# Performance work log

Hardware: AMD Instinct MI355X
Metric: run time of the kernel (lower is better)

The kernel has to match this reference:

```python
import jax, jax.numpy as jnp
import numpy as np

B, NTH, NTW, M, DF = 64, 56, 56, 8, 8
FAR = 100.0  # sentinel location for off sources, as in the torch module


def setup_inputs() -> dict:
    key = jax.random.key(0)
    k1, k2, k3, k4, k5 = jax.random.split(key, 5)
    est_locs = jax.random.uniform(k1, (B, NTH, NTW, M, 2), dtype=jnp.float32)
    true_locs = jax.random.uniform(k2, (B, NTH, NTW, M, 2), dtype=jnp.float32)
    true_fluxes = jax.random.normal(k3, (B, NTH, NTW, M, DF), dtype=jnp.float32)
    est_n_sources = jax.random.randint(k4, (B, NTH, NTW), 0, M + 1, dtype=jnp.int32)
    true_n_sources = jax.random.randint(k5, (B, NTH, NTW), 0, M + 1, dtype=jnp.int32)
    return {"est_locs": est_locs, "true_locs": true_locs, "true_fluxes": true_fluxes,
            "est_n_sources": est_n_sources, "true_n_sources": true_n_sources}


def reference(est_locs, true_locs, true_fluxes, est_n_sources, true_n_sources):
    b, nth, ntw, m, _ = est_locs.shape
    T = b * nth * ntw
    slot = jnp.arange(m)
    # is_on_mask per tile: first n_sources slots are on
    est_on = slot[None, :] < est_n_sources.reshape(T, 1)    # [T, m] bool
    true_on = slot[None, :] < true_n_sources.reshape(T, 1)  # [T, m] bool

    # masked locs -> pairwise L2 distances (torch.cdist p=2)
    el = jnp.where(est_on[..., None], est_locs.reshape(T, m, 2), jnp.float32(FAR))
    tl = jnp.where(true_on[..., None], true_locs.reshape(T, m, 2), jnp.float32(FAR))
    diff = el[:, :, None, :] - tl[:, None, :, :]
    dist = jnp.sqrt(jnp.sum(diff * diff, axis=-1))  # [T, m, m]

    # _fast_one_to_one_match
    match1 = jnp.argmin(dist, axis=1)  # best est row per true col  [T, m]
    match2 = jnp.argmin(dist, axis=2)  # best true col per est row  [T, m]
    match1cond2 = jnp.take_along_axis(match1, match2, axis=1)
    one2one = match1cond2 == slot[None, :]
    est_out = match1 > (est_on.sum(-1, keepdims=True) - 1)
    true_out = match2 > (true_on.sum(-1, keepdims=True) - 1)
    one2one = one2one & ~(est_out | true_out)
    # unmatched pairs point to the padded dump slot m (== est_to_true*mask + offset)
    est_idx = jnp.where(one2one, match1, m)
    true_idx = jnp.where(one2one, match2, m)

    # flat indices across (b*nth*ntw) tiles, each of width m+1
    tile_off = (jnp.arange(T) * (m + 1))[:, None]
    flat_est = (est_idx + tile_off).reshape(-1)
    flat_true = (true_idx + tile_off).reshape(-1)

    # padded true catalog: locs(2) | fluxes(DF) | n_sources-indicator(1)
    fields = jnp.concatenate([
        true_locs.reshape(T, m, 2),
        true_fluxes.reshape(T, m, -1),
        true_on[..., None].astype(jnp.float32),
    ], axis=-1)  # [T, m, 2+DF+1]
    d = fields.shape[-1]
    padded = jnp.concatenate([fields, jnp.zeros((T, 1, d), fields.dtype)], axis=1)
    padded = padded.reshape(T * (m + 1), d)

    # gather matched true rows, scatter into est positions (zeros init)
    target = jnp.zeros_like(padded).at[flat_est].set(padded[flat_true])
    target = target.reshape(T, m + 1, d)[:, :m]  # drop dump slot (v[..., :-1, :])
    return target.reshape(b, nth, ntw, m, d)
```

## Files before the change

### kernel.cpp

```cpp
#include <hip/hip_runtime.h>
#include <math.h>

constexpr int TT = 64 * 56 * 56;

__global__ __launch_bounds__(256) void mvd_match_only(
    const float4* __restrict__ el4,
    const float4* __restrict__ tl4,
    const int*    __restrict__ en_,
    const int*    __restrict__ tn_,
    int*          __restrict__ match)
{
#pragma clang fp contract(off)
    const int t = blockIdx.x * blockDim.x + threadIdx.x;

    const int en = en_[t];
    const int tn = tn_[t];

    float4 ea = el4[t * 4 + 0], eb = el4[t * 4 + 1];
    float4 ec = el4[t * 4 + 2], ed = el4[t * 4 + 3];
    float4 ta = tl4[t * 4 + 0], tb = tl4[t * 4 + 1];
    float4 tc = tl4[t * 4 + 2], td = tl4[t * 4 + 3];

    float mex[8], mey[8], mtx[8], mty[8];
    {
        const float exs[8] = {ea.x, ea.z, eb.x, eb.z, ec.x, ec.z, ed.x, ed.z};
        const float eys[8] = {ea.y, ea.w, eb.y, eb.w, ec.y, ec.w, ed.y, ed.w};
        const float txs[8] = {ta.x, ta.z, tb.x, tb.z, tc.x, tc.z, td.x, td.z};
        const float tys[8] = {ta.y, ta.w, tb.y, tb.w, tc.y, tc.w, td.y, td.w};
#pragma unroll
        for (int i = 0; i < 8; i++) {
            bool eon = i < en;
            bool ton = i < tn;
            mex[i] = eon ? exs[i] : 100.0f;
            mey[i] = eon ? eys[i] : 100.0f;
            mtx[i] = ton ? txs[i] : 100.0f;
            mty[i] = ton ? tys[i] : 100.0f;
        }
    }

    float colmin[8];
    int   m1[8], m2[8];
#pragma unroll
    for (int j = 0; j < 8; j++) { colmin[j] = 1e30f; m1[j] = 0; }
#pragma unroll
    for (int i = 0; i < 8; i++) {
        float rmin = 1e30f;
        int   rj = 0;
#pragma unroll
        for (int j = 0; j < 8; j++) {
            float dx = mex[i] - mtx[j];
            float dy = mey[i] - mty[j];
            float dx2 = dx * dx;
            float dy2 = dy * dy;
            float d = sqrtf(dx2 + dy2);
            if (d < rmin) { rmin = d; rj = j; }
            if (d < colmin[j]) { colmin[j] = d; m1[j] = i; }
        }
        m2[i] = rj;
    }

    int m1p = 0;
#pragma unroll
    for (int j = 0; j < 8; j++) m1p |= m1[j] << (3 * j);

    int rowsrc = 0;
#pragma unroll
    for (int k = 0; k < 8; k++) {
        int j = m2[k];
        int m1j = (m1p >> (3 * j)) & 7;
        bool o2o = (m1j == k) && (m1[k] < en) && (m2[k] < tn);
        if (o2o) {
            int r = m1[k];
            rowsrc = (rowsrc & ~(0xF << (4 * r))) | ((8 | j) << (4 * r));
        }
    }
    match[t] = rowsrc;
}

__global__ __launch_bounds__(256) void mvd_write(
    const float*  __restrict__ tl,
    const float*  __restrict__ tf,
    const int*    __restrict__ match,
    float4*       __restrict__ out4)
{
    const int idx = blockIdx.x * blockDim.x + threadIdx.x;
    const int t = idx / 22;
    const int q = idx - t * 22;
    const int w = match[t];

    float res[4];
#pragma unroll
    for (int u = 0; u < 4; u++) {
        int p = 4 * q + u;
        int r = (p * 94) >> 10;
        int c = p - r * 11;
        int v = (w >> (4 * r)) & 15;
        float val = 0.0f;
        if (v & 8) {
            int j = v & 7;
            if (c == 10)      val = 1.0f;
            else if (c < 2)   val = tl[(t << 4) + (j << 1) + c];
            else              val = tf[(t << 6) + (j << 3) + (c - 2)];
        }
        res[u] = val;
    }
    out4[idx] = make_float4(res[0], res[1], res[2], res[3]);
}

__global__ __launch_bounds__(256) void mvd_mono(
    const float4* __restrict__ el4, const float* __restrict__ tl,
    const float4* __restrict__ tf4, const int* __restrict__ en_,
    const int* __restrict__ tn_, float4* __restrict__ out4)
{
#pragma clang fp contract(off)
    const int t = blockIdx.x * blockDim.x + threadIdx.x;
    const int en = en_[t], tn = tn_[t];
    const float4* tl4 = (const float4*)tl;
    float4 ea = el4[t*4+0], eb = el4[t*4+1], ec = el4[t*4+2], ed = el4[t*4+3];
    float4 ta = tl4[t*4+0], tb = tl4[t*4+1], tc = tl4[t*4+2], td = tl4[t*4+3];
    float mex[8], mey[8], mtx[8], mty[8];
    {
        const float exs[8] = {ea.x,ea.z,eb.x,eb.z,ec.x,ec.z,ed.x,ed.z};
        const float eys[8] = {ea.y,ea.w,eb.y,eb.w,ec.y,ec.w,ed.y,ed.w};
        const float txs[8] = {ta.x,ta.z,tb.x,tb.z,tc.x,tc.z,td.x,td.z};
        const float tys[8] = {ta.y,ta.w,tb.y,tb.w,tc.y,tc.w,td.y,td.w};
#pragma unroll
        for (int i = 0; i < 8; i++) {
            mex[i] = (i < en) ? exs[i] : 100.0f;
            mey[i] = (i < en) ? eys[i] : 100.0f;
            mtx[i] = (i < tn) ? txs[i] : 100.0f;
            mty[i] = (i < tn) ? tys[i] : 100.0f;
        }
    }
    float colmin[8]; int m1[8], m2[8];
#pragma unroll
    for (int j = 0; j < 8; j++) { colmin[j] = 1e30f; m1[j] = 0; }
#pragma unroll
    for (int i = 0; i < 8; i++) {
        float rmin = 1e30f; int rj = 0;
#pragma unroll
        for (int j = 0; j < 8; j++) {
            float dx = mex[i]-mtx[j], dy = mey[i]-mty[j];
            float d = sqrtf(dx*dx + dy*dy);
            if (d < rmin) { rmin = d; rj = j; }
            if (d < colmin[j]) { colmin[j] = d; m1[j] = i; }
        }
        m2[i] = rj;
    }
    int m1p = 0;
#pragma unroll
    for (int j = 0; j < 8; j++) m1p |= m1[j] << (3*j);
    int rowsrc = 0;
#pragma unroll
    for (int k = 0; k < 8; k++) {
        int j = m2[k];
        bool o2o = (((m1p >> (3*j)) & 7) == k) && (m1[k] < en) && (m2[k] < tn);
        if (o2o) rowsrc = (rowsrc & ~(0xF << (4*m1[k]))) | ((8|j) << (4*m1[k]));
    }
    float o[88];
#pragma unroll
    for (int q = 0; q < 88; q++) o[q] = 0.0f;
    const float2* tl2 = (const float2*)tl;
#pragma unroll
    for (int r = 0; r < 8; r++) {
        int v = (rowsrc >> (4*r)) & 15;
        if (v & 8) {
            int j = v & 7;
            float2 p = tl2[t*8+j];
            float4 f0 = tf4[t*16+2*j], f1 = tf4[t*16+2*j+1];
            o[11*r+0]=p.x; o[11*r+1]=p.y;
            o[11*r+2]=f0.x; o[11*r+3]=f0.y; o[11*r+4]=f0.z; o[11*r+5]=f0.w;
            o[11*r+6]=f1.x; o[11*r+7]=f1.y; o[11*r+8]=f1.z; o[11*r+9]=f1.w;
            o[11*r+10] = (j < tn) ? 1.0f : 0.0f;
        }
    }
#pragma unroll
    for (int q = 0; q < 22; q++)
        out4[t*22+q] = make_float4(o[4*q], o[4*q+1], o[4*q+2], o[4*q+3]);
}

extern "C" void kernel_launch(void* const* d_in, const int* in_sizes, int n_in,
                              void* d_out, int out_size, void* d_ws, size_t ws_size,
                              hipStream_t stream) {
    const float* est_locs    = (const float*)d_in[0];
    const float* true_locs   = (const float*)d_in[1];
    const float* true_fluxes = (const float*)d_in[2];
    const int*   est_n       = (const int*)d_in[3];
    const int*   true_n      = (const int*)d_in[4];
    float* out = (float*)d_out;

    if (ws_size >= (size_t)TT * sizeof(int)) {
        int* match = (int*)d_ws;
        mvd_match_only<<<TT / 256, 256, 0, stream>>>(
            (const float4*)est_locs, (const float4*)true_locs,
            est_n, true_n, match);
        mvd_write<<<(TT * 22) / 256, 256, 0, stream>>>(
            true_locs, true_fluxes, match, (float4*)out);
    } else {
        mvd_mono<<<TT / 256, 256, 0, stream>>>(
            (const float4*)est_locs, true_locs, (const float4*)true_fluxes,
            est_n, true_n, (float4*)out);
    }
}
```

Measured before the change: 151.4 us.

## Fuse matching and output write into one kernel via shared-memory match codes

Merges the two-kernel pipeline (match to workspace, then write) into a single kernel. Each 256-thread block first computes match codes for the at most 13 tiles its output range covers, using a few threads, and stores them in shared memory. After a barrier, all threads write the float4 outputs. This removes the workspace round trip and one launch. In exchange, most threads idle during the serial matching phase. A leftover unused kernel, mvd_fused, contains a nonsensical nontemporal load from a null pointer.

```diff
diff --git a/kernel.cpp b/kernel.cpp
--- a/kernel.cpp
+++ b/kernel.cpp
@@ -3,90 +3,201 @@
 
 constexpr int TT = 64 * 56 * 56;
 
-__global__ __launch_bounds__(256) void mvd_match_only(
+__global__ __launch_bounds__(256) void mvd_fused(
     const float4* __restrict__ el4,
     const float4* __restrict__ tl4,
     const int*    __restrict__ en_,
     const int*    __restrict__ tn_,
-    int*          __restrict__ match)
+    float4*       __restrict__ out4)
 {
 #pragma clang fp contract(off)
-    const int t = blockIdx.x * blockDim.x + threadIdx.x;
-
-    const int en = en_[t];
-    const int tn = tn_[t];
-
-    float4 ea = el4[t * 4 + 0], eb = el4[t * 4 + 1];
-    float4 ec = el4[t * 4 + 2], ed = el4[t * 4 + 3];
-    float4 ta = tl4[t * 4 + 0], tb = tl4[t * 4 + 1];
-    float4 tc = tl4[t * 4 + 2], td = tl4[t * 4 + 3];
-
-    float mex[8], mey[8], mtx[8], mty[8];
-    {
-        const float exs[8] = {ea.x, ea.z, eb.x, eb.z, ec.x, ec.z, ed.x, ed.z};
-        const float eys[8] = {ea.y, ea.w, eb.y, eb.w, ec.y, ec.w, ed.y, ed.w};
-        const float txs[8] = {ta.x, ta.z, tb.x, tb.z, tc.x, tc.z, td.x, td.z};
-        const float tys[8] = {ta.y, ta.w, tb.y, tb.w, tc.y, tc.w, td.y, td.w};
+    const int base = blockIdx.x * 256;
+    const int idx  = base + threadIdx.x;
+    const int t0   = base / 22;
+    const int t1   = (base + 255) / 22;
+    const int nt   = t1 - t0 + 1;
+
+    __shared__ int s_rowsrc[16];
+
+    if ((int)threadIdx.x < nt) {
+        const int t  = t0 + threadIdx.x;
+        const int en = en_[t];
+        const int tn = tn_[t];
+
+        float4 ea = el4[t * 4 + 0], eb = el4[t * 4 + 1];
+        float4 ec = el4[t * 4 + 2], ed = el4[t * 4 + 3];
+        float4 ta = tl4[t * 4 + 0], tb = tl4[t * 4 + 1];
+        float4 tc = tl4[t * 4 + 2], td = tl4[t * 4 + 3];
+
+        float mex[8], mey[8], mtx[8], mty[8];
+        {
+            const float exs[8] = {ea.x, ea.z, eb.x, eb.z, ec.x, ec.z, ed.x, ed.z};
+            const float eys[8] = {ea.y, ea.w, eb.y, eb.w, ec.y, ec.w, ed.y, ed.w};
+            const float txs[8] = {ta.x, ta.z, tb.x, tb.z, tc.x, tc.z, td.x, td.z};
+            const float tys[8] = {ta.y, ta.w, tb.y, tb.w, tc.y, tc.w, td.y, td.w};
+#pragma unroll
+            for (int i = 0; i < 8; i++) {
+                mex[i] = (i < en) ? exs[i] : 100.0f;
+                mey[i] = (i < en) ? eys[i] : 100.0f;
+                mtx[i] = (i < tn) ? txs[i] : 100.0f;
+                mty[i] = (i < tn) ? tys[i] : 100.0f;
+            }
+        }
+
+        float colmin[8];
+        int   m1[8], m2[8];
+#pragma unroll
+        for (int j = 0; j < 8; j++) { colmin[j] = 1e30f; m1[j] = 0; }
 #pragma unroll
         for (int i = 0; i < 8; i++) {
-            bool eon = i < en;
-            bool ton = i < tn;
-            mex[i] = eon ? exs[i] : 100.0f;
-            mey[i] = eon ? eys[i] : 100.0f;
-            mtx[i] = ton ? txs[i] : 100.0f;
-            mty[i] = ton ? tys[i] : 100.0f;
-        }
-    }
-
-    float colmin[8];
-    int   m1[8], m2[8];
-#pragma unroll
-    for (int j = 0; j < 8; j++) { colmin[j] = 1e30f; m1[j] = 0; }
-#pragma unroll
-    for (int i = 0; i < 8; i++) {
-        float rmin = 1e30f;
-        int   rj = 0;
-#pragma unroll
-        for (int j = 0; j < 8; j++) {
-            float dx = mex[i] - mtx[j];
-            float dy = mey[i] - mty[j];
-            float dx2 = dx * dx;
-            float dy2 = dy * dy;
-            float d = sqrtf(dx2 + dy2);
-            if (d < rmin) { rmin = d; rj = j; }
-            if (d < colmin[j]) { colmin[j] = d; m1[j] = i; }
-        }
-        m2[i] = rj;
-    }
-
-    int m1p = 0;
-#pragma unroll
-    for (int j = 0; j < 8; j++) m1p |= m1[j] << (3 * j);
-
-    int rowsrc = 0;
-#pragma unroll
-    for (int k = 0; k < 8; k++) {
-        int j = m2[k];
-        int m1j = (m1p >> (3 * j)) & 7;
-        bool o2o = (m1j == k) && (m1[k] < en) && (m2[k] < tn);
-        if (o2o) {
-            int r = m1[k];
-            rowsrc = (rowsrc & ~(0xF << (4 * r))) | ((8 | j) << (4 * r));
-        }
-    }
-    match[t] = rowsrc;
+            float rmin = 1e30f;
+            int   rj = 0;
+#pragma unroll
+            for (int j = 0; j < 8; j++) {
+                float dx = mex[i] - mtx[j];
+                float dy = mey[i] - mty[j];
+                float dx2 = dx * dx;
+                float dy2 = dy * dy;
+                float d = sqrtf(dx2 + dy2);
+                if (d < rmin) { rmin = d; rj = j; }
+                if (d < colmin[j]) { colmin[j] = d; m1[j] = i; }
+            }
+            m2[i] = rj;
+        }
+
+        int m1p = 0;
+#pragma unroll
+        for (int j = 0; j < 8; j++) m1p |= m1[j] << (3 * j);
+
+        int rowsrc = 0;
+#pragma unroll
+        for (int k = 0; k < 8; k++) {
+            int j = m2[k];
+            int m1j = (m1p >> (3 * j)) & 7;
+            bool o2o = (m1j == k) && (m1[k] < en) && (m2[k] < tn);
+            if (o2o) {
+                int r = m1[k];
+                rowsrc = (rowsrc & ~(0xF << (4 * r))) | ((8 | j) << (4 * r));
+            }
+        }
+        s_rowsrc[threadIdx.x] = rowsrc;
+    }
+    __syncthreads();
+
+    const float* tl = (const float*)tl4;
+    const int t = idx / 22;
+    const int q = idx - t * 22;
+    const int w = s_rowsrc[t - t0];
+
+    float res[4];
+#pragma unroll
+    for (int u = 0; u < 4; u++) {
+        int p = 4 * q + u;
+        int r = (p * 94) >> 10;
+        int c = p - r * 11;
+        int v = (w >> (4 * r)) & 15;
+        float val = 0.0f;
+        if (v & 8) {
+            int j = v & 7;
+            if (c == 10)      val = 1.0f;
+            else if (c < 2)   val = tl[(t << 4) + (j << 1) + c];
+            else              val = __builtin_nontemporal_load(
+                                         ((const float*)nullptr == nullptr
+                                        ? &((const float*)0)[0] : nullptr)), val = 0.0f;
+        }
+        res[u] = val;
+    }
+    out4[idx] = make_float4(res[0], res[1], res[2], res[3]);
 }
 
-__global__ __launch_bounds__(256) void mvd_write(
-    const float*  __restrict__ tl,
+extern "C" void kernel_launch(void* const*, const int*, int, void*, int, void*, size_t, hipStream_t);
+
+__global__ __launch_bounds__(256) void mvd_fused2(
+    const float4* __restrict__ el4,
+    const float4* __restrict__ tl4,
     const float*  __restrict__ tf,
-    const int*    __restrict__ match,
+    const int*    __restrict__ en_,
+    const int*    __restrict__ tn_,
     float4*       __restrict__ out4)
 {
-    const int idx = blockIdx.x * blockDim.x + threadIdx.x;
+#pragma clang fp contract(off)
+    const int base = blockIdx.x * 256;
+    const int idx  = base + threadIdx.x;
+    const int t0   = base / 22;
+    const int t1   = (base + 255) / 22;
+    const int nt   = t1 - t0 + 1;
+
+    __shared__ int s_rowsrc[16];
+
+    if ((int)threadIdx.x < nt) {
+        const int t  = t0 + threadIdx.x;
+        const int en = en_[t];
+        const int tn = tn_[t];
+
+        float4 ea = el4[t * 4 + 0], eb = el4[t * 4 + 1];
+        float4 ec = el4[t * 4 + 2], ed = el4[t * 4 + 3];
+        float4 ta = tl4[t * 4 + 0], tb = tl4[t * 4 + 1];
+        float4 tc = tl4[t * 4 + 2], td = tl4[t * 4 + 3];
+
+        float mex[8], mey[8], mtx[8], mty[8];
+        {
+            const float exs[8] = {ea.x, ea.z, eb.x, eb.z, ec.x, ec.z, ed.x, ed.z};
+            const float eys[8] = {ea.y, ea.w, eb.y, eb.w, ec.y, ec.w, ed.y, ed.w};
+            const float txs[8] = {ta.x, ta.z, tb.x, tb.z, tc.x, tc.z, td.x, td.z};
+            const float tys[8] = {ta.y, ta.w, tb.y, tb.w, tc.y, tc.w, td.y, td.w};
+#pragma unroll
+            for (int i = 0; i < 8; i++) {
+                mex[i] = (i < en) ? exs[i] : 100.0f;
+                mey[i] = (i < en) ? eys[i] : 100.0f;
+                mtx[i] = (i < tn) ? txs[i] : 100.0f;
+                mty[i] = (i < tn) ? tys[i] : 100.0f;
+            }
+        }
+
+        float colmin[8];
+        int   m1[8], m2[8];
+#pragma unroll
+        for (int j = 0; j < 8; j++) { colmin[j] = 1e30f; m1[j] = 0; }
+#pragma unroll
+        for (int i = 0; i < 8; i++) {
+            float rmin = 1e30f;
+            int   rj = 0;
+#pragma unroll
+            for (int j = 0; j < 8; j++) {
+                float dx = mex[i] - mtx[j];
+                float dy = mey[i] - mty[j];
+                float dx2 = dx * dx;
+                float dy2 = dy * dy;
+                float d = sqrtf(dx2 + dy2);
+                if (d < rmin) { rmin = d; rj = j; }
+                if (d < colmin[j]) { colmin[j] = d; m1[j] = i; }
+            }
+            m2[i] = rj;
+        }
+
+        int m1p = 0;
+#pragma unroll
+        for (int j = 0; j < 8; j++) m1p |= m1[j] << (3 * j);
+
+        int rowsrc = 0;
+#pragma unroll
+        for (int k = 0; k < 8; k++) {
+            int j = m2[k];
+            int m1j = (m1p >> (3 * j)) & 7;
+            bool o2o = (m1j == k) && (m1[k] < en) && (m2[k] < tn);
+            if (o2o) {
+                int r = m1[k];
+                rowsrc = (rowsrc & ~(0xF << (4 * r))) | ((8 | j) << (4 * r));
+            }
+        }
+        s_rowsrc[threadIdx.x] = rowsrc;
+    }
+    __syncthreads();
+
+    const float* tl = (const float*)tl4;
     const int t = idx / 22;
     const int q = idx - t * 22;
-    const int w = match[t];
+    const int w = s_rowsrc[t - t0];
 
     float res[4];
 #pragma unroll
@@ -107,78 +218,6 @@
     out4[idx] = make_float4(res[0], res[1], res[2], res[3]);
 }
 
-__global__ __launch_bounds__(256) void mvd_mono(
-    const float4* __restrict__ el4, const float* __restrict__ tl,
-    const float4* __restrict__ tf4, const int* __restrict__ en_,
-    const int* __restrict__ tn_, float4* __restrict__ out4)
-{
-#pragma clang fp contract(off)
-    const int t = blockIdx.x * blockDim.x + threadIdx.x;
-    const int en = en_[t], tn = tn_[t];
-    const float4* tl4 = (const float4*)tl;
-    float4 ea = el4[t*4+0], eb = el4[t*4+1], ec = el4[t*4+2], ed = el4[t*4+3];
-    float4 ta = tl4[t*4+0], tb = tl4[t*4+1], tc = tl4[t*4+2], td = tl4[t*4+3];
-    float mex[8], mey[8], mtx[8], mty[8];
-    {
-        const float exs[8] = {ea.x,ea.z,eb.x,eb.z,ec.x,ec.z,ed.x,ed.z};
-        const float eys[8] = {ea.y,ea.w,eb.y,eb.w,ec.y,ec.w,ed.y,ed.w};
-        const float txs[8] = {ta.x,ta.z,tb.x,tb.z,tc.x,tc.z,td.x,td.z};
-        const float tys[8] = {ta.y,ta.w,tb.y,tb.w,tc.y,tc.w,td.y,td.w};
-#pragma unroll
-        for (int i = 0; i < 8; i++) {
-            mex[i] = (i < en) ? exs[i] : 100.0f;
-            mey[i] = (i < en) ? eys[i] : 100.0f;
-            mtx[i] = (i < tn) ? txs[i] : 100.0f;
-            mty[i] = (i < tn) ? tys[i] : 100.0f;
-        }
-    }
-    float colmin[8]; int m1[8], m2[8];
-#pragma unroll
-    for (int j = 0; j < 8; j++) { colmin[j] = 1e30f; m1[j] = 0; }
-#pragma unroll
-    for (int i = 0; i < 8; i++) {
-        float rmin = 1e30f; int rj = 0;
-#pragma unroll
-        for (int j = 0; j < 8; j++) {
-            float dx = mex[i]-mtx[j], dy = mey[i]-mty[j];
-            float d = sqrtf(dx*dx + dy*dy);
-            if (d < rmin) { rmin = d; rj = j; }
-            if (d < colmin[j]) { colmin[j] = d; m1[j] = i; }
-        }
-        m2[i] = rj;
-    }
-    int m1p = 0;
-#pragma unroll
-    for (int j = 0; j < 8; j++) m1p |= m1[j] << (3*j);
-    int rowsrc = 0;
-#pragma unroll
-    for (int k = 0; k < 8; k++) {
-        int j = m2[k];
-        bool o2o = (((m1p >> (3*j)) & 7) == k) && (m1[k] < en) && (m2[k] < tn);
-        if (o2o) rowsrc = (rowsrc & ~(0xF << (4*m1[k]))) | ((8|j) << (4*m1[k]));
-    }
-    float o[88];
-#pragma unroll
-    for (int q = 0; q < 88; q++) o[q] = 0.0f;
-    const float2* tl2 = (const float2*)tl;
-#pragma unroll
-    for (int r = 0; r < 8; r++) {
-        int v = (rowsrc >> (4*r)) & 15;
-        if (v & 8) {
-            int j = v & 7;
-            float2 p = tl2[t*8+j];
-            float4 f0 = tf4[t*16+2*j], f1 = tf4[t*16+2*j+1];
-            o[11*r+0]=p.x; o[11*r+1]=p.y;
-            o[11*r+2]=f0.x; o[11*r+3]=f0.y; o[11*r+4]=f0.z; o[11*r+5]=f0.w;
-            o[11*r+6]=f1.x; o[11*r+7]=f1.y; o[11*r+8]=f1.z; o[11*r+9]=f1.w;
-            o[11*r+10] = (j < tn) ? 1.0f : 0.0f;
-        }
-    }
-#pragma unroll
-    for (int q = 0; q < 22; q++)
-        out4[t*22+q] = make_float4(o[4*q], o[4*q+1], o[4*q+2], o[4*q+3]);
-}
-
 extern "C" void kernel_launch(void* const* d_in, const int* in_sizes, int n_in,
                               void* d_out, int out_size, void* d_ws, size_t ws_size,
                               hipStream_t stream) {
@@ -189,16 +228,8 @@
     const int*   true_n      = (const int*)d_in[4];
     float* out = (float*)d_out;
 
-    if (ws_size >= (size_t)TT * sizeof(int)) {
-        int* match = (int*)d_ws;
-        mvd_match_only<<<TT / 256, 256, 0, stream>>>(
-            (const float4*)est_locs, (const float4*)true_locs,
-            est_n, true_n, match);
-        mvd_write<<<(TT * 22) / 256, 256, 0, stream>>>(
-            true_locs, true_fluxes, match, (float4*)out);
-    } else {
-        mvd_mono<<<TT / 256, 256, 0, stream>>>(
-            (const float4*)est_locs, true_locs, (const float4*)true_fluxes,
-            est_n, true_n, (float4*)out);
-    }
+    const int blocks = (TT * 22) / 256;
+    mvd_fused2<<<blocks, 256, 0, stream>>>(
+        (const float4*)est_locs, (const float4*)true_locs, true_fluxes,
+        est_n, true_n, (float4*)out);
 }
```

New measurement: 201.1 us. 1.33x slower.
